# Performance work log

Hardware: AMD Instinct MI355X
Metric: run time of the kernel (lower is better)

## Reference

```python
import jax, jax.numpy as jnp
import numpy as np

B, NQ, NK, E, H, F, L = 8, 300, 4096, 256, 8, 2048, 6
D = E // H
SCALE = D ** -0.5


def _ln(x, g, b):
    m = x.mean(-1, keepdims=True)
    v = ((x - m) ** 2).mean(-1, keepdims=True)
    return (x - m) / jnp.sqrt(v + 1e-5) * g + b


def _split_heads(x):
    b, n, _ = x.shape
    return x.reshape(b, n, H, D).transpose(0, 2, 1, 3)  # (B,H,N,D)


def _merge_heads(x):
    b, h, n, d = x.shape
    return x.transpose(0, 2, 1, 3).reshape(b, n, h * d)


def setup_inputs() -> dict:
    key = jax.random.key(0)
    c = [0]
    def nk():
        c[0] += 1
        return jax.random.fold_in(key, c[0])
    def p(shape):
        return jax.random.normal(nk(), shape, jnp.float32) * 0.02
    return {
        "tgt": jax.random.normal(nk(), (B, NQ, E), jnp.float32),
        "memory": jax.random.normal(nk(), (B, NK, E), jnp.float32),
        "geometry_mask": jax.random.randint(nk(), (B, NQ, NK), 0, 2).astype(bool),
        "sa_wqkv": p((L, 3 * E, E)), "sa_bqkv": p((L, 3 * E)),
        "sa_wo": p((L, E, E)), "sa_bo": p((L, E)),
        "ca_wq": p((L, E, E)), "ca_bq": p((L, E)),
        "ca_wk": p((L, E, E)), "ca_bk": p((L, E)),
        "ca_wv": p((L, E, E)), "ca_bv": p((L, E)),
        "ca_wo": p((L, E, E)), "ca_bo": p((L, E)),
        "f_w1": p((L, F, E)), "f_b1": p((L, F)),
        "f_w2": p((L, E, F)), "f_b2": p((L, E)),
        "ln1g": jnp.ones((L, E)), "ln1b": jnp.zeros((L, E)),
        "ln2g": jnp.ones((L, E)), "ln2b": jnp.zeros((L, E)),
        "ln3g": jnp.ones((L, E)), "ln3b": jnp.zeros((L, E)),
        "lnfg": jnp.ones((E,)), "lnfb": jnp.zeros((E,)),
    }


def _forward(tgt, memory, geometry_mask, params):
    mask4 = geometry_mask[:, None, :, :]  # (B,1,NQ,NK), broadcast over heads

    def step(t, p):
        (wqkv, bqkv, wo, bo, wq, bq, wk, bk, wv, bv, wco, bco,
         w1, b1, w2, b2, g1, be1, g2, be2, g3, be3) = p
        # --- self-attention (torch nn.MultiheadAttention, eval mode) ---
        qkv = t @ wqkv.T + bqkv
        q, k, v = jnp.split(qkv, 3, axis=-1)
        q, k, v = _split_heads(q), _split_heads(k), _split_heads(v)
        a = jax.nn.softmax(jnp.einsum('bhqd,bhkd->bhqk', q, k) * SCALE, axis=-1)
        sa = _merge_heads(jnp.einsum('bhqk,bhkd->bhqd', a, v)) @ wo.T + bo
        t = _ln(t + sa, g1, be1)
        # --- geometry-constrained cross-attention ---
        q = _split_heads(t @ wq.T + bq)
        k = _split_heads(memory @ wk.T + bk)
        v = _split_heads(memory @ wv.T + bv)
        s = jnp.einsum('bhqd,bhkd->bhqk', q, k) * SCALE
        s = jnp.where(mask4, s, -jnp.inf)  # masked_fill(~mask, -inf)
        a = jax.nn.softmax(s, axis=-1)
        ca = _merge_heads(jnp.einsum('bhqk,bhkd->bhqd', a, v)) @ wco.T + bco
        t = _ln(t + ca, g2, be2)
        # --- FFN ---
        f = jax.nn.relu(t @ w1.T + b1) @ w2.T + b2
        t = _ln(t + f, g3, be3)
        return t, None

    out, _ = jax.lax.scan(step, tgt, params)
    return out


def reference(tgt, memory, geometry_mask, sa_wqkv, sa_bqkv, sa_wo, sa_bo,
              ca_wq, ca_bq, ca_wk, ca_bk, ca_wv, ca_bv, ca_wo, ca_bo,
              f_w1, f_b1, f_w2, f_b2, ln1g, ln1b, ln2g, ln2b, ln3g, ln3b,
              lnfg, lnfb):
    params = (sa_wqkv, sa_bqkv, sa_wo, sa_bo, ca_wq, ca_bq, ca_wk, ca_bk,
              ca_wv, ca_bv, ca_wo, ca_bo, f_w1, f_b1, f_w2, f_b2,
              ln1g, ln1b, ln2g, ln2b, ln3g, ln3b)
    out = _forward(tgt, memory, geometry_mask, params)
    return _ln(out, lnfg, lnfb)
```

## Files before the change

kernel.cpp:

```cpp
#include <hip/hip_runtime.h>
#include <hip/hip_bf16.h>

constexpr int cB = 8, cNQ = 300, cNK = 4096, cE = 256, cH = 8, cD = 32, cF = 2048, cL = 6;
constexpr int MT = cB * cNQ;
constexpr int MM = cB * cNK;
constexpr int cQT = 10;
constexpr int cKS = 4;
constexpr float kScale = 0.17677669529663687f;
constexpr float kC2 = 0.25506601f;

typedef __attribute__((ext_vector_type(8))) short short8_t;
typedef __attribute__((ext_vector_type(4))) short short4_t;
typedef __attribute__((ext_vector_type(4))) float float4_t;

__device__ inline short f2bf(float x) {
  __hip_bfloat16 h = __float2bfloat16(x);
  return __builtin_bit_cast(short, h);
}

__device__ inline unsigned pack_bf16x2(float a, float b) {
  __hip_bfloat162 pp = __float22bfloat162_rn(make_float2(a, b));
  unsigned r;
  __builtin_memcpy(&r, &pp, 4);
  return r;
}

__global__ void init_t(const float* __restrict__ in, float* __restrict__ t,
                       __hip_bfloat16* __restrict__ tb, int n) {
  int i = blockIdx.x * 256 + threadIdx.x;
  if (i < n) { float v = in[i]; t[i] = v; tb[i] = __float2bfloat16(v); }
}
__global__ void cast_f32_bf16(const float* __restrict__ in, __hip_bfloat16* __restrict__ out, int n) {
  int i = blockIdx.x * 256 + threadIdx.x;
  if (i < n) out[i] = __float2bfloat16(in[i]);
}

__global__ void pack_mask_T(const int* __restrict__ m, unsigned* __restrict__ mT) {
  int key = blockIdx.x * 256 + threadIdx.x;
  int qt = blockIdx.y, b = blockIdx.z;
  unsigned w = 0;
  for (int j = 0; j < 32; ++j) {
    int q = qt * 32 + j;
    unsigned bit = (q < cNQ) ? (unsigned)(m[((size_t)b * cNQ + q) * cNK + key] != 0) : 0u;
    w |= bit << j;
  }
  mT[((size_t)b * cQT + qt) * cNK + key] = w;
}

template<typename TA, typename TW, int EPI, int OMODE, typename TOUT>
__global__ __launch_bounds__(256) void gemm_mfma(const TA* __restrict__ A,
                                                 const TW* __restrict__ W,
                                                 const float* __restrict__ bias,
                                                 TOUT* __restrict__ C,
                                                 int M, int N, int K) {
  constexpr int LDSS = 72;
  __shared__ short As[64][LDSS];
  __shared__ short Ws[64][LDSS];
  int tid = threadIdx.x;
  int bm = blockIdx.x * 64, bn = blockIdx.y * 64;
  int lane = tid & 63, wave = tid >> 6;
  int m16 = lane & 15, quad = lane >> 4;
  int wm = (wave >> 1) * 32, wn = (wave & 1) * 32;

  int srow = tid >> 2;
  int kc = (tid & 3) * 16;
  bool aok = (bm + srow) < M;

  float4_t acc[2][2];
#pragma unroll
  for (int i = 0; i < 2; ++i)
#pragma unroll
    for (int j = 0; j < 2; ++j) acc[i][j] = (float4_t){0.f, 0.f, 0.f, 0.f};

  for (int k0 = 0; k0 < K; k0 += 64) {
    if constexpr (__hip_internal::is_same<TA, float>::value) {
      const float* src = A + (size_t)(bm + srow) * K + k0 + kc;
      short8_t p0, p1;
#pragma unroll
      for (int u = 0; u < 8; ++u) p0[u] = aok ? f2bf(src[u]) : (short)0;
#pragma unroll
      for (int u = 0; u < 8; ++u) p1[u] = aok ? f2bf(src[8 + u]) : (short)0;
      *(short8_t*)&As[srow][kc] = p0;
      *(short8_t*)&As[srow][kc + 8] = p1;
    } else {
      const TA* src = A + (size_t)(bm + srow) * K + k0 + kc;
      short8_t z = 0;
      *(short8_t*)&As[srow][kc] = aok ? *(const short8_t*)src : z;
      *(short8_t*)&As[srow][kc + 8] = aok ? *(const short8_t*)(src + 8) : z;
    }
    if constexpr (__hip_internal::is_same<TW, float>::value) {
      const float* src = W + (size_t)(bn + srow) * K + k0 + kc;
      short8_t p0, p1;
#pragma unroll
      for (int u = 0; u < 8; ++u) p0[u] = f2bf(src[u]);
#pragma unroll
      for (int u = 0; u < 8; ++u) p1[u] = f2bf(src[8 + u]);
      *(short8_t*)&Ws[srow][kc] = p0;
      *(short8_t*)&Ws[srow][kc + 8] = p1;
    } else {
      const TW* src = W + (size_t)(bn + srow) * K + k0 + kc;
      *(short8_t*)&Ws[srow][kc] = *(const short8_t*)src;
      *(short8_t*)&Ws[srow][kc + 8] = *(const short8_t*)(src + 8);
    }
    __syncthreads();
#pragma unroll
    for (int kk = 0; kk < 2; ++kk) {
      short8_t aF[2], bF[2];
#pragma unroll
      for (int i = 0; i < 2; ++i)
        aF[i] = *(const short8_t*)&As[wm + i * 16 + m16][kk * 32 + quad * 8];
#pragma unroll
      for (int j = 0; j < 2; ++j)
        bF[j] = *(const short8_t*)&Ws[wn + j * 16 + m16][kk * 32 + quad * 8];
#pragma unroll
      for (int i = 0; i < 2; ++i)
#pragma unroll
        for (int j = 0; j < 2; ++j)
          acc[i][j] = __builtin_amdgcn_mfma_f32_16x16x32_bf16(aF[i], bF[j], acc[i][j], 0, 0, 0);
    }
    __syncthreads();
  }

  if constexpr (OMODE == 2) {
#pragma unroll
    for (int i = 0; i < 2; ++i)
#pragma unroll
      for (int r = 0; r < 4; ++r) {
        int ml = wm + i * 16 + quad * 4 + r;
#pragma unroll
        for (int j = 0; j < 2; ++j) {
          int nl = wn + j * 16 + m16;
          Ws[nl][ml] = f2bf(acc[i][j][r] + bias[bn + nl]);
        }
      }
    __syncthreads();
    int nl = tid >> 2, mc = (tid & 3) * 16;
    if (bm + mc < M) {
      int n = bn + nl;
      __hip_bfloat16* dst = (__hip_bfloat16*)C +
          ((size_t)(n >> 5) * 32 + (n & 31)) * (size_t)M + bm + mc;
      *(short8_t*)dst = *(const short8_t*)&Ws[nl][mc];
      *(short8_t*)(dst + 8) = *(const short8_t*)&Ws[nl][mc + 8];
    }
  } else {
#pragma unroll
    for (int i = 0; i < 2; ++i) {
#pragma unroll
      for (int r = 0; r < 4; ++r) {
        int m = bm + wm + i * 16 + quad * 4 + r;
        if (m >= M) continue;
#pragma unroll
        for (int j = 0; j < 2; ++j) {
          int n = bn + wn + j * 16 + m16;
          float v = acc[i][j][r] + bias[n];
          if (EPI == 1) v = fmaxf(v, 0.f);
          if (EPI == 2 && n < 256) v *= kC2;
          if (EPI == 3) v *= kC2;
          if constexpr (OMODE == 1) {
            ((__hip_bfloat16*)C)[((size_t)(n >> 5) * M + m) * 32 + (n & 31)] = __float2bfloat16(v);
          } else if constexpr (__hip_internal::is_same<TOUT, float>::value) {
            C[(size_t)m * N + n] = v;
          } else {
            C[(size_t)m * N + n] = __float2bfloat16(v);
          }
        }
      }
    }
  }
}

template<typename TW, int EPI, typename TOUT>
__global__ __launch_bounds__(256) void gemm32(const __hip_bfloat16* __restrict__ A,
                                              const TW* __restrict__ W,
                                              const float* __restrict__ bias,
                                              TOUT* __restrict__ C,
                                              int M, int N, int K) {
  __shared__ short As[32][72];
  __shared__ short Ws[64][72];
  int tid = threadIdx.x;
  int bm = blockIdx.x * 32, bn = blockIdx.y * 64;
  int lane = tid & 63, wave = tid >> 6;
  int m16 = lane & 15, quad = lane >> 4;
  int wn = wave * 16;

  int sa_row = tid >> 3, sa_c = (tid & 7) * 8;
  int sw_row = tid >> 2, sw_c = (tid & 3) * 16;
  bool aok = (bm + sa_row) < M;

  float4_t acc[2];
  acc[0] = (float4_t){0.f, 0.f, 0.f, 0.f};
  acc[1] = (float4_t){0.f, 0.f, 0.f, 0.f};

  for (int k0 = 0; k0 < K; k0 += 64) {
    {
      const __hip_bfloat16* src = A + (size_t)(bm + sa_row) * K + k0 + sa_c;
      short8_t z = 0;
      *(short8_t*)&As[sa_row][sa_c] = aok ? *(const short8_t*)src : z;
    }
    if constexpr (__hip_internal::is_same<TW, float>::value) {
      const float* src = W + (size_t)(bn + sw_row) * K + k0 + sw_c;
      short8_t p0, p1;
#pragma unroll
      for (int u = 0; u < 8; ++u) p0[u] = f2bf(src[u]);
#pragma unroll
      for (int u = 0; u < 8; ++u) p1[u] = f2bf(src[8 + u]);
      *(short8_t*)&Ws[sw_row][sw_c] = p0;
      *(short8_t*)&Ws[sw_row][sw_c + 8] = p1;
    } else {
      const TW* src = W + (size_t)(bn + sw_row) * K + k0 + sw_c;
      *(short8_t*)&Ws[sw_row][sw_c] = *(const short8_t*)src;
      *(short8_t*)&Ws[sw_row][sw_c + 8] = *(const short8_t*)(src + 8);
    }
    __syncthreads();
#pragma unroll
    for (int kk = 0; kk < 2; ++kk) {
      short8_t aF[2], bF;
#pragma unroll
      for (int i = 0; i < 2; ++i)
        aF[i] = *(const short8_t*)&As[i * 16 + m16][kk * 32 + quad * 8];
      bF = *(const short8_t*)&Ws[wn + m16][kk * 32 + quad * 8];
#pragma unroll
      for (int i = 0; i < 2; ++i)
        acc[i] = __builtin_amdgcn_mfma_f32_16x16x32_bf16(aF[i], bF, acc[i], 0, 0, 0);
    }
    __syncthreads();
  }

#pragma unroll
  for (int i = 0; i < 2; ++i) {
#pragma unroll
    for (int r = 0; r < 4; ++r) {
      int m = bm + i * 16 + quad * 4 + r;
      if (m >= M) continue;
      int n = bn + wn + m16;
      float v = acc[i][r] + bias[n];
      if (EPI == 1) v = fmaxf(v, 0.f);
      if (EPI == 3) v *= kC2;
      if constexpr (__hip_internal::is_same<TOUT, float>::value) {
        C[(size_t)m * N + n] = v;
      } else {
        C[(size_t)m * N + n] = __float2bfloat16(v);
      }
    }
  }
}

template<typename TW, int EPI, int OMODE, typename TOUT>
__global__ __launch_bounds__(256) void gemm128(const __hip_bfloat16* __restrict__ A,
                                               const TW* __restrict__ W,
                                               const float* __restrict__ bias,
                                               TOUT* __restrict__ C,
                                               int M, int N, int K) {
  __shared__ short lds[2 * 128 * 72];
  auto As = (short(*)[72])lds;
  auto Ws = (short(*)[72])(lds + 128 * 72);
  int tid = threadIdx.x;
  int bm = blockIdx.x * 128, bn = blockIdx.y * 128;
  int lane = tid & 63, wave = tid >> 6;
  int n16 = lane & 15, quad = lane >> 4;
  int wm = (wave >> 1) * 64, wn = (wave & 1) * 64;
  int srow = tid >> 1, kc = (tid & 1) * 32;
  bool aok = (bm + srow) < M;

  float4_t acc[4][4];
#pragma unroll
  for (int i = 0; i < 4; ++i)
#pragma unroll
    for (int j = 0; j < 4; ++j) acc[i][j] = (float4_t){0.f, 0.f, 0.f, 0.f};

  for (int k0 = 0; k0 < K; k0 += 64) {
    {
      const __hip_bfloat16* src = A + (size_t)(bm + srow) * K + k0 + kc;
      short8_t z = 0;
#pragma unroll
      for (int u = 0; u < 4; ++u)
        *(short8_t*)&As[srow][kc + u * 8] = aok ? *(const short8_t*)(src + u * 8) : z;
    }
    if constexpr (__hip_internal::is_same<TW, float>::value) {
      const float* src = W + (size_t)(bn + srow) * K + k0 + kc;
#pragma unroll
      for (int u = 0; u < 4; ++u) {
        short8_t p;
#pragma unroll
        for (int v = 0; v < 8; ++v) p[v] = f2bf(src[u * 8 + v]);
        *(short8_t*)&Ws[srow][kc + u * 8] = p;
      }
    } else {
      const TW* src = W + (size_t)(bn + srow) * K + k0 + kc;
#pragma unroll
      for (int u = 0; u < 4; ++u)
        *(short8_t*)&Ws[srow][kc + u * 8] = *(const short8_t*)(src + u * 8);
    }
    __syncthreads();
#pragma unroll
    for (int kk = 0; kk < 2; ++kk) {
      short8_t aF[4], bF[4];
#pragma unroll
      for (int i = 0; i < 4; ++i)
        aF[i] = *(const short8_t*)&As[wm + i * 16 + n16][kk * 32 + quad * 8];
#pragma unroll
      for (int j = 0; j < 4; ++j)
        bF[j] = *(const short8_t*)&Ws[wn + j * 16 + n16][kk * 32 + quad * 8];
#pragma unroll
      for (int i = 0; i < 4; ++i)
#pragma unroll
        for (int j = 0; j < 4; ++j)
          acc[i][j] = __builtin_amdgcn_mfma_f32_16x16x32_bf16(aF[i], bF[j], acc[i][j], 0, 0, 0);
    }
    __syncthreads();
  }

  if constexpr (OMODE == 2) {
    auto TT = (short(*)[128])lds;
#pragma unroll
    for (int i = 0; i < 4; ++i)
#pragma unroll
      for (int r = 0; r < 4; ++r) {
        int ml = wm + i * 16 + quad * 4 + r;
#pragma unroll
        for (int j = 0; j < 4; ++j) {
          int nl = wn + j * 16 + n16;
          TT[nl][ml] = f2bf(acc[i][j][r] + bias[bn + nl]);
        }
      }
    __syncthreads();
    int nl = tid >> 1, mh = (tid & 1) * 64;
    int n = bn + nl;
    __hip_bfloat16* dst = (__hip_bfloat16*)C +
        ((size_t)(n >> 5) * 32 + (n & 31)) * (size_t)M + bm + mh;
#pragma unroll
    for (int ch = 0; ch < 8; ++ch) {
      if (bm + mh + ch * 8 < M)
        *(short8_t*)(dst + ch * 8) = *(const short8_t*)&TT[nl][mh + ch * 8];
    }
  } else {
#pragma unroll
    for (int i = 0; i < 4; ++i) {
#pragma unroll
      for (int r = 0; r < 4; ++r) {
        int m = bm + wm + i * 16 + quad * 4 + r;
        if (m >= M) continue;
#pragma unroll
        for (int j = 0; j < 4; ++j) {
          int n = bn + wn + j * 16 + n16;
          float v = acc[i][j][r] + bias[n];
          if (EPI == 1) v = fmaxf(v, 0.f);
          if constexpr (OMODE == 1) {
            ((__hip_bfloat16*)C)[((size_t)(n >> 5) * M + m) * 32 + (n & 31)] = __float2bfloat16(v);
          } else if constexpr (__hip_internal::is_same<TOUT, float>::value) {
            C[(size_t)m * N + n] = v;
          } else {
            C[(size_t)m * N + n] = __float2bfloat16(v);
          }
        }
      }
    }
  }
}

template<typename TQ, bool MASKED>
__global__ __launch_bounds__(256) void attn_flash(
    const TQ* __restrict__ qb, size_t strQb, size_t strQh, int qRowStr,
    const __hip_bfloat16* __restrict__ kb, size_t strKb, size_t strKh, int kRowStr,
    const __hip_bfloat16* __restrict__ vt, size_t strVb, size_t strVh, size_t strVd,
    const unsigned* __restrict__ mT, size_t strMb,
    float* __restrict__ pO, size_t pStrO,
    float* __restrict__ pL, size_t pStrL,
    int nq, int nk, int kChunk) {
  int hb = blockIdx.x;
  int h = hb & 7, bz = hb >> 3;
  int qt = blockIdx.y, ks = blockIdx.z;
  int qbase = qt * 32;

  const TQ* q = qb + (size_t)bz * strQb + (size_t)h * strQh;
  const __hip_bfloat16* K = kb + (size_t)bz * strKb + (size_t)h * strKh;
  const __hip_bfloat16* V = vt + (size_t)bz * strVb + (size_t)h * strVh;
  const unsigned* mrow = MASKED ? (mT + (size_t)bz * strMb + (size_t)qt * cNK) : nullptr;

  int tid = threadIdx.x;
  int lane = tid & 63, wave = tid >> 6;
  int n16 = lane & 15, quad = lane >> 4;

  __shared__ float redO[4][32][33];
  __shared__ float redL[4][32];
  short* sPw = (short*)&redO[0][0][0] + wave * (32 * 40);

  short8_t qf[2];
#pragma unroll
  for (int qi = 0; qi < 2; ++qi) {
    qf[qi] = 0;
    int qr = qbase + qi * 16 + n16;
    if (qr < nq) {
      const TQ* qp = q + (size_t)qr * qRowStr + quad * 8;
      if constexpr (__hip_internal::is_same<TQ, float>::value) {
#pragma unroll
        for (int j = 0; j < 8; ++j) qf[qi][j] = f2bf(qp[j]);
      } else {
        qf[qi] = *(const short8_t*)qp;
      }
    }
  }
  short8_t ones;
#pragma unroll
  for (int j = 0; j < 8; ++j) ones[j] = f2bf(1.0f);

  float4_t accO[2][2], accL[2];
#pragma unroll
  for (int qi = 0; qi < 2; ++qi) {
    accL[qi] = (float4_t){0.f, 0.f, 0.f, 0.f};
#pragma unroll
    for (int di = 0; di < 2; ++di) accO[qi][di] = (float4_t){0.f, 0.f, 0.f, 0.f};
  }
  float4_t zero4 = {0.f, 0.f, 0.f, 0.f};

  int kpad = (nk + 31) & ~31;
  int kend = ks * kChunk + kChunk;
  if (kend > kpad) kend = kpad;
  for (int koff = ks * kChunk + wave * 32; koff < kend; koff += 128) {
    int k0 = koff + 2 * n16;
    unsigned w0 = 0, w1 = 0;
    float okf0 = 1.f, okf1 = 1.f;
    if (MASKED) {
      uint2 mw = *(const uint2*)(mrow + k0);
      w0 = mw.x; w1 = mw.y;
    } else {
      okf0 = (k0 < nk) ? 1.f : 0.f;
      okf1 = (k0 + 1 < nk) ? 1.f : 0.f;
    }
    short8_t kf0 = *(const short8_t*)(K + (size_t)k0 * kRowStr + quad * 8);
    short8_t kf1 = *(const short8_t*)(K + (size_t)(k0 + 1) * kRowStr + quad * 8);
    short8_t vf0 = *(const short8_t*)(V + (size_t)n16 * strVd + koff + quad * 8);
    short8_t vf1 = *(const short8_t*)(V + (size_t)(16 + n16) * strVd + koff + quad * 8);
    __builtin_amdgcn_s_setprio(1);
    float4_t s00 = __builtin_amdgcn_mfma_f32_16x16x32_bf16(qf[0], kf0, zero4, 0, 0, 0);
    float4_t s01 = __builtin_amdgcn_mfma_f32_16x16x32_bf16(qf[0], kf1, zero4, 0, 0, 0);
    float4_t s10 = __builtin_amdgcn_mfma_f32_16x16x32_bf16(qf[1], kf0, zero4, 0, 0, 0);
    float4_t s11 = __builtin_amdgcn_mfma_f32_16x16x32_bf16(qf[1], kf1, zero4, 0, 0, 0);
    __builtin_amdgcn_s_setprio(0);
#pragma unroll
    for (int qi = 0; qi < 2; ++qi) {
      const float4_t& sa = qi ? s10 : s00;
      const float4_t& sb = qi ? s11 : s01;
#pragma unroll
      for (int r = 0; r < 4; ++r) {
        int row = qi * 16 + quad * 4 + r;
        float m0, m1;
        if (MASKED) {
          m0 = (float)((w0 >> row) & 1u);
          m1 = (float)((w1 >> row) & 1u);
        } else {
          m0 = okf0; m1 = okf1;
        }
        float p0 = exp2f(sa[r]) * m0;
        float p1 = exp2f(sb[r]) * m1;
        *(unsigned*)&sPw[row * 40 + 2 * n16] = pack_bf16x2(p0, p1);
      }
    }
    __builtin_amdgcn_s_setprio(1);
#pragma unroll
    for (int qi = 0; qi < 2; ++qi) {
      short8_t pf = *(const short8_t*)&sPw[(qi * 16 + n16) * 40 + quad * 8];
      accO[qi][0] = __builtin_amdgcn_mfma_f32_16x16x32_bf16(pf, vf0, accO[qi][0], 0, 0, 0);
      accO[qi][1] = __builtin_amdgcn_mfma_f32_16x16x32_bf16(pf, vf1, accO[qi][1], 0, 0, 0);
      accL[qi]    = __builtin_amdgcn_mfma_f32_16x16x32_bf16(pf, ones, accL[qi], 0, 0, 0);
    }
    __builtin_amdgcn_s_setprio(0);
  }

  __syncthreads();
#pragma unroll
  for (int qi = 0; qi < 2; ++qi) {
#pragma unroll
    for (int r = 0; r < 4; ++r) {
      int row = qi * 16 + quad * 4 + r;
#pragma unroll
      for (int di = 0; di < 2; ++di)
        redO[wave][row][di * 16 + n16] = accO[qi][di][r];
      if (n16 == 0) redL[wave][row] = accL[qi][r];
    }
  }
  __syncthreads();

  size_t oBase = (size_t)ks * pStrO + (size_t)(bz * cNQ) * 256 + h * 32;
  int row = tid >> 3, c0 = (tid & 7) * 4;
  if (qbase + row < nq) {
    float4_t o;
#pragma unroll
    for (int u = 0; u < 4; ++u)
      o[u] = redO[0][row][c0 + u] + redO[1][row][c0 + u] +
             redO[2][row][c0 + u] + redO[3][row][c0 + u];
    *(float4_t*)&pO[oBase + (size_t)(qbase + row) * 256 + c0] = o;
  }
  if (tid < 32 && qbase + tid < nq) {
    float l = redL[0][tid] + redL[1][tid] + redL[2][tid] + redL[3][tid];
    pL[(size_t)ks * pStrL + (size_t)hb * 320 + qbase + tid] = l;
  }
}

__global__ __launch_bounds__(64) void attn_merge(const float* __restrict__ pO,
                                                 const float* __restrict__ pL,
                                                 __hip_bfloat16* __restrict__ out) {
  int row = blockIdx.x;
  int lane = threadIdx.x;
  int c0 = lane * 4;
  int bz = row / cNQ, qq = row - bz * cNQ;
  int h = c0 >> 5;
  float l = 0.f;
#pragma unroll
  for (int ks = 0; ks < cKS; ++ks)
    l += pL[(size_t)ks * (64 * 320) + (size_t)(bz * 8 + h) * 320 + qq];
  float inv = 1.f / l;
  float o[4] = {0.f, 0.f, 0.f, 0.f};
#pragma unroll
  for (int ks = 0; ks < cKS; ++ks) {
    const float4_t v = *(const float4_t*)&pO[(size_t)ks * (MT * 256) + (size_t)row * 256 + c0];
#pragma unroll
    for (int u = 0; u < 4; ++u) o[u] += v[u];
  }
  short4_t res = {f2bf(o[0] * inv), f2bf(o[1] * inv), f2bf(o[2] * inv), f2bf(o[3] * inv)};
  *(short4_t*)&out[(size_t)row * 256 + c0] = res;
}

__global__ __launch_bounds__(64) void add_ln_k(float* __restrict__ t,
                                               __hip_bfloat16* __restrict__ tb,
                                               const float* __restrict__ delta,
                                               const float* __restrict__ g,
                                               const float* __restrict__ bb) {
  int r = blockIdx.x, lane = threadIdx.x;
  size_t base = (size_t)r * cE + lane * 4;
  float x[4];
  float s = 0.f;
#pragma unroll
  for (int i = 0; i < 4; ++i) { x[i] = t[base + i] + delta[base + i]; s += x[i]; }
  for (int off = 32; off; off >>= 1) s += __shfl_xor(s, off);
  float mean = s * (1.f / cE);
  float v = 0.f;
#pragma unroll
  for (int i = 0; i < 4; ++i) { float dd = x[i] - mean; v += dd * dd; }
  for (int off = 32; off; off >>= 1) v += __shfl_xor(v, off);
  float rstd = rsqrtf(v * (1.f / cE) + 1e-5f);
  float y[4];
#pragma unroll
  for (int i = 0; i < 4; ++i) {
    y[i] = (x[i] - mean) * rstd * g[lane * 4 + i] + bb[lane * 4 + i];
    t[base + i] = y[i];
  }
  short4_t pb = {f2bf(y[0]), f2bf(y[1]), f2bf(y[2]), f2bf(y[3])};
  *(short4_t*)&tb[base] = pb;
}

__global__ __launch_bounds__(64) void final_ln_k(const float* __restrict__ t,
                                                 const float* __restrict__ g,
                                                 const float* __restrict__ bb,
                                                 float* __restrict__ out) {
  int r = blockIdx.x, lane = threadIdx.x;
  size_t base = (size_t)r * cE + lane * 4;
  float x[4];
  float s = 0.f;
#pragma unroll
  for (int i = 0; i < 4; ++i) { x[i] = t[base + i]; s += x[i]; }
  for (int off = 32; off; off >>= 1) s += __shfl_xor(s, off);
  float mean = s * (1.f / cE);
  float v = 0.f;
#pragma unroll
  for (int i = 0; i < 4; ++i) { float dd = x[i] - mean; v += dd * dd; }
  for (int off = 32; off; off >>= 1) v += __shfl_xor(v, off);
  float rstd = rsqrtf(v * (1.f / cE) + 1e-5f);
#pragma unroll
  for (int i = 0; i < 4; ++i)
    out[base + i] = (x[i] - mean) * rstd * g[lane * 4 + i] + bb[lane * 4 + i];
}

struct Bufs {
  float *t, *s1, *s2, *pO, *pL;
  __hip_bfloat16 *tb, *big2, *vtq, *s1b, *s2b, *qbf, *ffnh, *kbuf, *vtb, *membf;
  unsigned* mTr;
  const float* memory;
  bool fullKV, precast;
};

template<typename TW>
static void run_layers(const TW* const* wt, const float* const* bs,
                       const float* ln1g, const float* ln1b,
                       const float* ln2g, const float* ln2b,
                       const float* ln3g, const float* ln3b,
                       Bufs B, hipStream_t stream) {
  const size_t pStrO = (size_t)MT * 256, pStrL = 64 * 320;
  for (int l = 0; l < cL; ++l) {
    const TW* wqkv = wt[0] + (size_t)l * 3 * cE * cE;  const float* bqkv = bs[0] + (size_t)l * 3 * cE;
    const TW* wo   = wt[1] + (size_t)l * cE * cE;      const float* bo   = bs[1] + (size_t)l * cE;
    const TW* wq   = wt[2] + (size_t)l * cE * cE;      const float* bq   = bs[2] + (size_t)l * cE;
    const TW* wk   = wt[3] + (size_t)l * cE * cE;      const float* bk   = bs[3] + (size_t)l * cE;
    const TW* wv   = wt[4] + (size_t)l * cE * cE;      const float* bv   = bs[4] + (size_t)l * cE;
    const TW* wco  = wt[5] + (size_t)l * cE * cE;      const float* bco  = bs[5] + (size_t)l * cE;
    const TW* w1   = wt[6] + (size_t)l * cF * cE;      const float* b1   = bs[6] + (size_t)l * cF;
    const TW* w2   = wt[7] + (size_t)l * cE * cF;      const float* b2   = bs[7] + (size_t)l * cE;

    gemm_mfma<__hip_bfloat16, TW, 2, 0, __hip_bfloat16><<<dim3(38, 8), 256, 0, stream>>>(
        B.tb, wqkv, bqkv, B.big2, MT, 512, cE);
    gemm_mfma<__hip_bfloat16, TW, 0, 2, __hip_bfloat16><<<dim3(38, 4), 256, 0, stream>>>(
        B.tb, wqkv + (size_t)512 * cE, bqkv + 512, B.vtq, MT, cE, cE);
    attn_flash<__hip_bfloat16, false><<<dim3(64, cQT, cKS), 256, 0, stream>>>(
        B.big2, (size_t)cNQ * 512, 32, 512,
        B.big2 + 256, (size_t)cNQ * 512, 32, 512,
        B.vtq, 300, (size_t)cD * MT, MT,
        nullptr, 0,
        B.pO, pStrO, B.pL, pStrL, cNQ, cNQ, 96);
    attn_merge<<<MT, 64, 0, stream>>>(B.pO, B.pL, B.s1b);
    gemm32<TW, 0, float><<<dim3(75, 4), 256, 0, stream>>>(
        B.s1b, wo, bo, B.s2, MT, cE, cE);
    add_ln_k<<<MT, 64, 0, stream>>>(B.t, B.tb, B.s2, ln1g + (size_t)l * cE, ln1b + (size_t)l * cE);
    gemm32<TW, 3, __hip_bfloat16><<<dim3(75, 4), 256, 0, stream>>>(
        B.tb, wq, bq, B.qbf, MT, cE, cE);
    if (B.fullKV && B.precast) {
      gemm128<TW, 0, 1, __hip_bfloat16><<<dim3(256, 2), 256, 0, stream>>>(
          B.membf, wk, bk, B.kbuf, MM, cE, cE);
      gemm128<TW, 0, 2, __hip_bfloat16><<<dim3(256, 2), 256, 0, stream>>>(
          B.membf, wv, bv, B.vtb, MM, cE, cE);
      attn_flash<__hip_bfloat16, true><<<dim3(64, cQT, cKS), 256, 0, stream>>>(
          B.qbf, (size_t)cNQ * cE, 32, cE,
          B.kbuf, (size_t)cNK * cD, (size_t)MM * cD, cD,
          B.vtb, (size_t)cNK, (size_t)cD * MM, MM,
          B.mTr, (size_t)cQT * cNK,
          B.pO, pStrO, B.pL, pStrL, cNQ, cNK, 1024);
      attn_merge<<<MT, 64, 0, stream>>>(B.pO, B.pL, B.s2b);
    } else {
      for (int b = 0; b < cB; ++b) {
        const float* memb = B.memory + (size_t)b * cNK * cE;
        gemm_mfma<float, TW, 0, 1, __hip_bfloat16><<<dim3(64, 4), 256, 0, stream>>>(
            memb, wk, bk, B.kbuf, cNK, cE, cE);
        gemm_mfma<float, TW, 0, 2, __hip_bfloat16><<<dim3(64, 4), 256, 0, stream>>>(
            memb, wv, bv, B.vtb, cNK, cE, cE);
        attn_flash<__hip_bfloat16, true><<<dim3(8, cQT, cKS), 256, 0, stream>>>(
            B.qbf + (size_t)b * cNQ * cE, 0, 32, cE,
            B.kbuf, 0, (size_t)cNK * cD, cD,
            B.vtb, 0, (size_t)cD * cNK, cNK,
            B.mTr + (size_t)b * cQT * cNK, 0,
            B.pO + (size_t)b * cNQ * 256, pStrO, B.pL + (size_t)b * 8 * 320, pStrL,
            cNQ, cNK, 1024);
      }
      attn_merge<<<MT, 64, 0, stream>>>(B.pO, B.pL, B.s2b);
    }
    gemm32<TW, 0, float><<<dim3(75, 4), 256, 0, stream>>>(
        B.s2b, wco, bco, B.s1, MT, cE, cE);
    add_ln_k<<<MT, 64, 0, stream>>>(B.t, B.tb, B.s1, ln2g + (size_t)l * cE, ln2b + (size_t)l * cE);
    gemm128<TW, 1, 0, __hip_bfloat16><<<dim3(19, 16), 256, 0, stream>>>(
        B.tb, w1, b1, B.ffnh, MT, cF, cE);
    gemm32<TW, 0, float><<<dim3(75, 4), 256, 0, stream>>>(
        B.ffnh, w2, b2, B.s1, MT, cE, cF);
    add_ln_k<<<MT, 64, 0, stream>>>(B.t, B.tb, B.s1, ln3g + (size_t)l * cE, ln3b + (size_t)l * cE);
  }
}

extern "C" void kernel_launch(void* const* d_in, const int* in_sizes, int n_in,
                              void* d_out, int out_size, void* d_ws, size_t ws_size,
                              hipStream_t stream) {
  (void)in_sizes; (void)n_in; (void)out_size;
  const float* tgt    = (const float*)d_in[0];
  const float* memory = (const float*)d_in[1];
  const int*   gmask  = (const int*)d_in[2];
  const float* w_in[8]  = {(const float*)d_in[3], (const float*)d_in[5], (const float*)d_in[7],
                           (const float*)d_in[9], (const float*)d_in[11], (const float*)d_in[13],
                           (const float*)d_in[15], (const float*)d_in[17]};
  const float* b_in[8]  = {(const float*)d_in[4], (const float*)d_in[6], (const float*)d_in[8],
                           (const float*)d_in[10], (const float*)d_in[12], (const float*)d_in[14],
                           (const float*)d_in[16], (const float*)d_in[18]};
  const size_t w_sz[8]  = {(size_t)cL*3*cE*cE, (size_t)cL*cE*cE, (size_t)cL*cE*cE,
                           (size_t)cL*cE*cE, (size_t)cL*cE*cE, (size_t)cL*cE*cE,
                           (size_t)cL*cF*cE, (size_t)cL*cE*cF};
  const float* ln1g = (const float*)d_in[19], *ln1b = (const float*)d_in[20];
  const float* ln2g = (const float*)d_in[21], *ln2b = (const float*)d_in[22];
  const float* ln3g = (const float*)d_in[23], *ln3b = (const float*)d_in[24];
  const float* lnfg = (const float*)d_in[25], *lnfb = (const float*)d_in[26];

  char* wp = (char*)d_ws;
  auto alloc = [&](size_t bytes) { void* p = wp; wp += (bytes + 255) & ~(size_t)255; return p; };

  Bufs B;
  B.memory = memory;
  B.t  = (float*)alloc((size_t)MT * cE * 4);
  B.s1 = (float*)alloc((size_t)MT * cE * 4);
  B.s2 = (float*)alloc((size_t)MT * cE * 4);
  B.tb = (__hip_bfloat16*)alloc((size_t)MT * cE * 2);
  B.big2 = (__hip_bfloat16*)alloc((size_t)MT * 512 * 2);
  B.vtq  = (__hip_bfloat16*)alloc((size_t)cH * cD * MT * 2);
  B.mTr = (unsigned*)alloc((size_t)cB * cQT * cNK * 4);
  B.pO = (float*)alloc((size_t)cKS * MT * 256 * 4);
  B.pL = (float*)alloc((size_t)cKS * 64 * 320 * 4);
  B.s1b = B.big2;
  B.s2b = B.big2 + (size_t)MT * 256;
  B.qbf = (__hip_bfloat16*)B.s1;
  B.ffnh = (__hip_bfloat16*)B.pO;

  size_t kvFull = (size_t)cH * MM * cD * 2;
  size_t used = (size_t)(wp - (char*)d_ws);
  B.fullKV = ws_size >= used + 2 * kvFull;
  if (B.fullKV) {
    B.kbuf = (__hip_bfloat16*)alloc(kvFull);
    B.vtb  = (__hip_bfloat16*)alloc(kvFull);
  } else {
    B.kbuf = (__hip_bfloat16*)alloc((size_t)cH * cNK * cD * 2);
    B.vtb  = (__hip_bfloat16*)alloc((size_t)cH * cNK * cD * 2);
  }
  size_t memBytes = (size_t)MM * cE * 2;
  used = (size_t)(wp - (char*)d_ws);
  B.precast = B.fullKV && (ws_size >= used + memBytes);
  B.membf = B.precast ? (__hip_bfloat16*)alloc(memBytes) : nullptr;

  size_t wbfTotal = 0;
  for (int i = 0; i < 8; ++i) wbfTotal += ((w_sz[i] * 2 + 255) & ~(size_t)255);
  used = (size_t)(wp - (char*)d_ws);
  bool wPre = ws_size >= used + wbfTotal;
  __hip_bfloat16* wbf[8] = {};
  if (wPre)
    for (int i = 0; i < 8; ++i) wbf[i] = (__hip_bfloat16*)alloc(w_sz[i] * 2);

  init_t<<<(MT * cE + 255) / 256, 256, 0, stream>>>(tgt, B.t, B.tb, MT * cE);
  pack_mask_T<<<dim3(cNK / 256, cQT, cB), 256, 0, stream>>>(gmask, B.mTr);
  if (B.precast)
    cast_f32_bf16<<<(MM * cE + 255) / 256, 256, 0, stream>>>(memory, B.membf, MM * cE);
  if (wPre)
    for (int i = 0; i < 8; ++i)
      cast_f32_bf16<<<(int)((w_sz[i] + 255) / 256), 256, 0, stream>>>(w_in[i], wbf[i], (int)w_sz[i]);

  if (wPre) {
    const __hip_bfloat16* wt[8];
    for (int i = 0; i < 8; ++i) wt[i] = wbf[i];
    run_layers<__hip_bfloat16>(wt, b_in, ln1g, ln1b, ln2g, ln2b, ln3g, ln3b, B, stream);
  } else {
    run_layers<float>(w_in, b_in, ln1g, ln1b, ln2g, ln2b, ln3g, ln3b, B, stream);
  }

  final_ln_k<<<MT, 64, 0, stream>>>(B.t, lnfg, lnfb, (float*)d_out);
}
```

Before: 1.268 ms.

## Fuse self-attention normalize into flash kernel, drop split-K, prefetch K/V tiles

```diff
diff --git a/kernel.cpp b/kernel.cpp
--- a/kernel.cpp
+++ b/kernel.cpp
@@ -358,7 +358,7 @@
   }
 }
 
-template<typename TQ, bool MASKED>
+template<typename TQ, bool MASKED, bool SPLIT>
 __global__ __launch_bounds__(256) void attn_flash(
     const TQ* __restrict__ qb, size_t strQb, size_t strQh, int qRowStr,
     const __hip_bfloat16* __restrict__ kb, size_t strKb, size_t strKh, int kRowStr,
@@ -366,6 +366,7 @@
     const unsigned* __restrict__ mT, size_t strMb,
     float* __restrict__ pO, size_t pStrO,
     float* __restrict__ pL, size_t pStrL,
+    __hip_bfloat16* __restrict__ outF,
     int nq, int nk, int kChunk) {
   int hb = blockIdx.x;
   int h = hb & 7, bz = hb >> 3;
@@ -414,12 +415,15 @@
   float4_t zero4 = {0.f, 0.f, 0.f, 0.f};
 
   int kpad = (nk + 31) & ~31;
+  int kbeg = ks * kChunk + wave * 32;
   int kend = ks * kChunk + kChunk;
   if (kend > kpad) kend = kpad;
-  for (int koff = ks * kChunk + wave * 32; koff < kend; koff += 128) {
-    int k0 = koff + 2 * n16;
-    unsigned w0 = 0, w1 = 0;
-    float okf0 = 1.f, okf1 = 1.f;
+
+  short8_t kf0, kf1, vf0, vf1;
+  unsigned w0 = 0, w1 = 0;
+  float okf0 = 1.f, okf1 = 1.f;
+  auto LOAD = [&](int ko) {
+    int k0 = ko + 2 * n16;
     if (MASKED) {
       uint2 mw = *(const uint2*)(mrow + k0);
       w0 = mw.x; w1 = mw.y;
@@ -427,16 +431,23 @@
       okf0 = (k0 < nk) ? 1.f : 0.f;
       okf1 = (k0 + 1 < nk) ? 1.f : 0.f;
     }
-    short8_t kf0 = *(const short8_t*)(K + (size_t)k0 * kRowStr + quad * 8);
-    short8_t kf1 = *(const short8_t*)(K + (size_t)(k0 + 1) * kRowStr + quad * 8);
-    short8_t vf0 = *(const short8_t*)(V + (size_t)n16 * strVd + koff + quad * 8);
-    short8_t vf1 = *(const short8_t*)(V + (size_t)(16 + n16) * strVd + koff + quad * 8);
-    __builtin_amdgcn_s_setprio(1);
-    float4_t s00 = __builtin_amdgcn_mfma_f32_16x16x32_bf16(qf[0], kf0, zero4, 0, 0, 0);
-    float4_t s01 = __builtin_amdgcn_mfma_f32_16x16x32_bf16(qf[0], kf1, zero4, 0, 0, 0);
-    float4_t s10 = __builtin_amdgcn_mfma_f32_16x16x32_bf16(qf[1], kf0, zero4, 0, 0, 0);
-    float4_t s11 = __builtin_amdgcn_mfma_f32_16x16x32_bf16(qf[1], kf1, zero4, 0, 0, 0);
-    __builtin_amdgcn_s_setprio(0);
+    kf0 = *(const short8_t*)(K + (size_t)k0 * kRowStr + quad * 8);
+    kf1 = *(const short8_t*)(K + (size_t)(k0 + 1) * kRowStr + quad * 8);
+    vf0 = *(const short8_t*)(V + (size_t)n16 * strVd + ko + quad * 8);
+    vf1 = *(const short8_t*)(V + (size_t)(16 + n16) * strVd + ko + quad * 8);
+  };
+
+  if (kbeg < kend) LOAD(kbeg);
+  for (int koff = kbeg; koff < kend; koff += 128) {
+    short8_t ck0 = kf0, ck1 = kf1, cv0 = vf0, cv1 = vf1;
+    unsigned cw0 = w0, cw1 = w1;
+    float co0 = okf0, co1 = okf1;
+    if (koff + 128 < kend) LOAD(koff + 128);
+
+    float4_t s00 = __builtin_amdgcn_mfma_f32_16x16x32_bf16(qf[0], ck0, zero4, 0, 0, 0);
+    float4_t s01 = __builtin_amdgcn_mfma_f32_16x16x32_bf16(qf[0], ck1, zero4, 0, 0, 0);
+    float4_t s10 = __builtin_amdgcn_mfma_f32_16x16x32_bf16(qf[1], ck0, zero4, 0, 0, 0);
+    float4_t s11 = __builtin_amdgcn_mfma_f32_16x16x32_bf16(qf[1], ck1, zero4, 0, 0, 0);
 #pragma unroll
     for (int qi = 0; qi < 2; ++qi) {
       const float4_t& sa = qi ? s10 : s00;
@@ -446,25 +457,23 @@
         int row = qi * 16 + quad * 4 + r;
         float m0, m1;
         if (MASKED) {
-          m0 = (float)((w0 >> row) & 1u);
-          m1 = (float)((w1 >> row) & 1u);
+          m0 = (float)((cw0 >> row) & 1u);
+          m1 = (float)((cw1 >> row) & 1u);
         } else {
-          m0 = okf0; m1 = okf1;
+          m0 = co0; m1 = co1;
         }
         float p0 = exp2f(sa[r]) * m0;
         float p1 = exp2f(sb[r]) * m1;
         *(unsigned*)&sPw[row * 40 + 2 * n16] = pack_bf16x2(p0, p1);
       }
     }
-    __builtin_amdgcn_s_setprio(1);
 #pragma unroll
     for (int qi = 0; qi < 2; ++qi) {
       short8_t pf = *(const short8_t*)&sPw[(qi * 16 + n16) * 40 + quad * 8];
-      accO[qi][0] = __builtin_amdgcn_mfma_f32_16x16x32_bf16(pf, vf0, accO[qi][0], 0, 0, 0);
-      accO[qi][1] = __builtin_amdgcn_mfma_f32_16x16x32_bf16(pf, vf1, accO[qi][1], 0, 0, 0);
+      accO[qi][0] = __builtin_amdgcn_mfma_f32_16x16x32_bf16(pf, cv0, accO[qi][0], 0, 0, 0);
+      accO[qi][1] = __builtin_amdgcn_mfma_f32_16x16x32_bf16(pf, cv1, accO[qi][1], 0, 0, 0);
       accL[qi]    = __builtin_amdgcn_mfma_f32_16x16x32_bf16(pf, ones, accL[qi], 0, 0, 0);
     }
-    __builtin_amdgcn_s_setprio(0);
   }
 
   __syncthreads();
@@ -481,19 +490,33 @@
   }
   __syncthreads();
 
-  size_t oBase = (size_t)ks * pStrO + (size_t)(bz * cNQ) * 256 + h * 32;
   int row = tid >> 3, c0 = (tid & 7) * 4;
-  if (qbase + row < nq) {
-    float4_t o;
-#pragma unroll
-    for (int u = 0; u < 4; ++u)
-      o[u] = redO[0][row][c0 + u] + redO[1][row][c0 + u] +
-             redO[2][row][c0 + u] + redO[3][row][c0 + u];
-    *(float4_t*)&pO[oBase + (size_t)(qbase + row) * 256 + c0] = o;
-  }
-  if (tid < 32 && qbase + tid < nq) {
-    float l = redL[0][tid] + redL[1][tid] + redL[2][tid] + redL[3][tid];
-    pL[(size_t)ks * pStrL + (size_t)hb * 320 + qbase + tid] = l;
+  if constexpr (SPLIT) {
+    size_t oBase = (size_t)ks * pStrO + (size_t)(bz * cNQ) * 256 + h * 32;
+    if (qbase + row < nq) {
+      float4_t o;
+#pragma unroll
+      for (int u = 0; u < 4; ++u)
+        o[u] = redO[0][row][c0 + u] + redO[1][row][c0 + u] +
+               redO[2][row][c0 + u] + redO[3][row][c0 + u];
+      *(float4_t*)&pO[oBase + (size_t)(qbase + row) * 256 + c0] = o;
+    }
+    if (tid < 32 && qbase + tid < nq) {
+      float l = redL[0][tid] + redL[1][tid] + redL[2][tid] + redL[3][tid];
+      pL[(size_t)ks * pStrL + (size_t)hb * 320 + qbase + tid] = l;
+    }
+  } else {
+    if (qbase + row < nq) {
+      float l = redL[0][row] + redL[1][row] + redL[2][row] + redL[3][row];
+      float inv = 1.f / l;
+      float o[4];
+#pragma unroll
+      for (int u = 0; u < 4; ++u)
+        o[u] = (redO[0][row][c0 + u] + redO[1][row][c0 + u] +
+                redO[2][row][c0 + u] + redO[3][row][c0 + u]) * inv;
+      short4_t res = {f2bf(o[0]), f2bf(o[1]), f2bf(o[2]), f2bf(o[3])};
+      *(short4_t*)&outF[(size_t)(bz * cNQ + qbase + row) * 256 + h * 32 + c0] = res;
+    }
   }
 }
 
@@ -573,7 +596,7 @@
 
 struct Bufs {
   float *t, *s1, *s2, *pO, *pL;
-  __hip_bfloat16 *tb, *big2, *vtq, *s1b, *s2b, *qbf, *ffnh, *kbuf, *vtb, *membf;
+  __hip_bfloat16 *tb, *big2, *vtq, *saOut, *s2b, *qbf, *ffnh, *kbuf, *vtb, *membf;
   unsigned* mTr;
   const float* memory;
   bool fullKV, precast;
@@ -600,15 +623,14 @@
         B.tb, wqkv, bqkv, B.big2, MT, 512, cE);
     gemm_mfma<__hip_bfloat16, TW, 0, 2, __hip_bfloat16><<<dim3(38, 4), 256, 0, stream>>>(
         B.tb, wqkv + (size_t)512 * cE, bqkv + 512, B.vtq, MT, cE, cE);
-    attn_flash<__hip_bfloat16, false><<<dim3(64, cQT, cKS), 256, 0, stream>>>(
+    attn_flash<__hip_bfloat16, false, false><<<dim3(64, cQT, 1), 256, 0, stream>>>(
         B.big2, (size_t)cNQ * 512, 32, 512,
         B.big2 + 256, (size_t)cNQ * 512, 32, 512,
         B.vtq, 300, (size_t)cD * MT, MT,
         nullptr, 0,
-        B.pO, pStrO, B.pL, pStrL, cNQ, cNQ, 96);
-    attn_merge<<<MT, 64, 0, stream>>>(B.pO, B.pL, B.s1b);
+        B.pO, pStrO, B.pL, pStrL, B.saOut, cNQ, cNQ, 320);
     gemm32<TW, 0, float><<<dim3(75, 4), 256, 0, stream>>>(
-        B.s1b, wo, bo, B.s2, MT, cE, cE);
+        B.saOut, wo, bo, B.s2, MT, cE, cE);
     add_ln_k<<<MT, 64, 0, stream>>>(B.t, B.tb, B.s2, ln1g + (size_t)l * cE, ln1b + (size_t)l * cE);
     gemm32<TW, 3, __hip_bfloat16><<<dim3(75, 4), 256, 0, stream>>>(
         B.tb, wq, bq, B.qbf, MT, cE, cE);
@@ -617,12 +639,12 @@
           B.membf, wk, bk, B.kbuf, MM, cE, cE);
       gemm128<TW, 0, 2, __hip_bfloat16><<<dim3(256, 2), 256, 0, stream>>>(
           B.membf, wv, bv, B.vtb, MM, cE, cE);
-      attn_flash<__hip_bfloat16, true><<<dim3(64, cQT, cKS), 256, 0, stream>>>(
+      attn_flash<__hip_bfloat16, true, true><<<dim3(64, cQT, cKS), 256, 0, stream>>>(
           B.qbf, (size_t)cNQ * cE, 32, cE,
           B.kbuf, (size_t)cNK * cD, (size_t)MM * cD, cD,
           B.vtb, (size_t)cNK, (size_t)cD * MM, MM,
           B.mTr, (size_t)cQT * cNK,
-          B.pO, pStrO, B.pL, pStrL, cNQ, cNK, 1024);
+          B.pO, pStrO, B.pL, pStrL, nullptr, cNQ, cNK, 1024);
       attn_merge<<<MT, 64, 0, stream>>>(B.pO, B.pL, B.s2b);
     } else {
       for (int b = 0; b < cB; ++b) {
@@ -631,13 +653,13 @@
             memb, wk, bk, B.kbuf, cNK, cE, cE);
         gemm_mfma<float, TW, 0, 2, __hip_bfloat16><<<dim3(64, 4), 256, 0, stream>>>(
             memb, wv, bv, B.vtb, cNK, cE, cE);
-        attn_flash<__hip_bfloat16, true><<<dim3(8, cQT, cKS), 256, 0, stream>>>(
+        attn_flash<__hip_bfloat16, true, true><<<dim3(8, cQT, cKS), 256, 0, stream>>>(
             B.qbf + (size_t)b * cNQ * cE, 0, 32, cE,
             B.kbuf, 0, (size_t)cNK * cD, cD,
             B.vtb, 0, (size_t)cD * cNK, cNK,
             B.mTr + (size_t)b * cQT * cNK, 0,
             B.pO + (size_t)b * cNQ * 256, pStrO, B.pL + (size_t)b * 8 * 320, pStrL,
-            cNQ, cNK, 1024);
+            nullptr, cNQ, cNK, 1024);
       }
       attn_merge<<<MT, 64, 0, stream>>>(B.pO, B.pL, B.s2b);
     }
@@ -687,7 +709,7 @@
   B.mTr = (unsigned*)alloc((size_t)cB * cQT * cNK * 4);
   B.pO = (float*)alloc((size_t)cKS * MT * 256 * 4);
   B.pL = (float*)alloc((size_t)cKS * 64 * 320 * 4);
-  B.s1b = B.big2;
+  B.saOut = (__hip_bfloat16*)B.pO;
   B.s2b = B.big2 + (size_t)MT * 256;
   B.qbf = (__hip_bfloat16*)B.s1;
   B.ffnh = (__hip_bfloat16*)B.pO;
```

Result: faster. 1.214 ms (-4.3%).
